# Kernel tuning notes

Measured on AMD Instinct MI355X. Metric: run time of the kernel, lower is better.

The kernel has to match this reference:

```python
import jax, jax.numpy as jnp
import numpy as np

TEMP = 0.1
W1, W2 = 0.5, 0.5
W3 = 1.0 - W1 - W2  # = 0.0, as in the original module defaults


def setup_inputs() -> dict:
    key = jax.random.key(0)
    ks = jax.random.split(key, 8)
    N, D = 131072, 256
    C1, C2, C3 = 1000, 100, 20
    features = jax.random.normal(ks[0], (N, D), dtype=jnp.float32) * 0.1
    prototypes_1 = jax.random.normal(ks[1], (C1, D), dtype=jnp.float32)
    labels_1 = jax.random.randint(ks[2], (N,), 0, C1)
    prototypes_2 = jax.random.normal(ks[3], (C2, D), dtype=jnp.float32)
    # ensure every coarse class appears (torch.unique == arange(C))
    labels_2 = jax.random.permutation(ks[4], jnp.arange(N) % C2)
    prototypes_3 = jax.random.normal(ks[5], (C3, D), dtype=jnp.float32)
    labels_3 = jax.random.permutation(ks[6], jnp.arange(N) % C3)
    return {
        "features": features,
        "prototypes_1": prototypes_1,
        "labels_1": labels_1,
        "prototypes_2": prototypes_2,
        "labels_2": labels_2,
        "prototypes_3": prototypes_3,
        "labels_3": labels_3,
    }


def _proto_nce(means, protos):
    # means: [C, D], protos: [C, D]; pos_mask(one_hot of unique=arange) is identity
    sim = (means @ protos.T) / TEMP              # [C, C]
    pos = jnp.diagonal(sim)                      # [C]
    return -jnp.mean(pos - jax.nn.logsumexp(sim, axis=1))


def _segment_mean(features, labels, num_segments):
    sums = jax.ops.segment_sum(features, labels, num_segments=num_segments)
    cnt = jax.ops.segment_sum(jnp.ones((labels.shape[0],), features.dtype),
                              labels, num_segments=num_segments)
    return sums / cnt[:, None]


def reference(features, prototypes_1, labels_1, prototypes_2, labels_2,
              prototypes_3, labels_3):
    # fine level: per-sample InfoNCE against fine prototypes
    fine_sim = (features @ prototypes_1.T) / TEMP            # [N, C1]
    fine_pos = jnp.take_along_axis(fine_sim, labels_1[:, None], axis=1)[:, 0]
    fine_loss = -jnp.mean(fine_pos - jax.nn.logsumexp(fine_sim, axis=1))

    # coarse level: per-class feature means (segment mean == masked-mean loop)
    coarse_means = _segment_mean(features, labels_2, prototypes_2.shape[0])
    coarse_loss = _proto_nce(coarse_means, prototypes_2)

    # con-coarse level
    con_means = _segment_mean(features, labels_3, prototypes_3.shape[0])
    con_coarse_loss = _proto_nce(con_means, prototypes_3)

    loss = W1 * fine_loss + W2 * coarse_loss + W3 * con_coarse_loss
    return (loss, fine_loss, coarse_loss, con_coarse_loss)
```

## Files before the change

kernel.cpp:

```cpp
#include <hip/hip_runtime.h>
#include <math.h>

#define WS_POS   0
#define WS_LSE   1
#define WS_ACC2  2
#define WS_ACC3  3
#define WS_S2    256
#define WS_S3    (256+25600)
#define WS_SEG   163840
#define NROWS    144
#define PART_FLOATS (NROWS*256 + 128)
#define PIMG_BYTE_OFF 131072

#define SC2  14.426950408889634f
#define BIAS 48.0f

typedef __attribute__((ext_vector_type(4))) float f32x4;
typedef __attribute__((ext_vector_type(8))) short short8;

static __device__ __forceinline__ unsigned f2bf(float f) {
    union { float f; unsigned u; } x; x.f = f;
    unsigned r = x.u + 0x7FFFu + ((x.u >> 16) & 1u);
    return r >> 16;
}

__global__ void k_zero(float* __restrict__ p, int count) {
    int i = blockIdx.x * 256 + threadIdx.x;
    if (i < count) p[i] = 0.f;
}

__global__ void k_prep(const float* __restrict__ p1, unsigned short* __restrict__ Pimg,
                       float* __restrict__ ws, int C1) {
    if (blockIdx.x == 0) ws[threadIdx.x] = 0.f;
    int e = blockIdx.x * 256 + threadIdx.x;
    int r  = e >> 5;
    int k0 = (e & 31) * 8;
    unsigned h[8];
#pragma unroll
    for (int j = 0; j < 8; ++j)
        h[j] = (r < C1) ? f2bf(p1[(size_t)r * 256 + k0 + j]) : 0u;
    uint4 v;
    v.x = h[0] | (h[1] << 16);
    v.y = h[2] | (h[3] << 16);
    v.z = h[4] | (h[5] << 16);
    v.w = h[6] | (h[7] << 16);
    *(uint4*)(Pimg + (size_t)r * 256 + k0) = v;
}

__global__ __launch_bounds__(256, 2) void k_seg(
        const float* __restrict__ feat, const float* __restrict__ p1,
        const int* __restrict__ l1, const int* __restrict__ l2,
        const int* __restrict__ l3, float* __restrict__ ws,
        int partMask, int useAtomic) {
    __shared__ int labs23[512];
    __shared__ int labs1[512];
    __shared__ float psum[4];
    const int tid  = threadIdx.x;
    const int lane = tid & 63;
    const int wv   = tid >> 6;
    const int g    = lane >> 4;
    const int rs   = lane & 15;
    const int chunk = blockIdx.x >> 1, half = blockIdx.x & 1;
    const int base  = chunk * 512;
    const int dimbase = half * 128 + wv * 32;

    for (int j = tid; j < 512; j += 256) {
        labs23[j] = l2[base + j] | (l3[base + j] << 16);
        labs1[j]  = l1[base + j];
    }
    __syncthreads();

    f32x4 acc[9][2];
#pragma unroll
    for (int mt = 0; mt < 9; ++mt)
#pragma unroll
        for (int nt = 0; nt < 2; ++nt) acc[mt][nt] = (f32x4){0.f, 0.f, 0.f, 0.f};

    float fA[16], pA[16], fB[16], pB[16];
    float posacc = 0.f;

#define LOADSTEP(u, F, P) { \
    const int sl0 = (u) * 32 + 8 * g; \
    _Pragma("unroll") \
    for (int j = 0; j < 8; ++j) { \
        const int sl = sl0 + j; \
        const size_t fb = (size_t)(base + sl) * 256 + dimbase + rs; \
        F[j]     = feat[fb]; \
        F[8 + j] = feat[fb + 16]; \
        const size_t pb = (size_t)labs1[sl] * 256 + dimbase + rs; \
        P[j]     = p1[pb]; \
        P[8 + j] = p1[pb + 16]; \
    } }

#define PROCSTEP(u, F, P) { \
    _Pragma("unroll") \
    for (int j = 0; j < 16; ++j) posacc = fmaf(F[j], P[j], posacc); \
    union { unsigned w[4]; short8 s; } b0, b1; \
    _Pragma("unroll") \
    for (int q = 0; q < 4; ++q) { \
        asm("v_cvt_pk_bf16_f32 %0, %1, %2" : "=v"(b0.w[q]) : "v"(F[2*q]),   "v"(F[2*q+1])); \
        asm("v_cvt_pk_bf16_f32 %0, %1, %2" : "=v"(b1.w[q]) : "v"(F[8+2*q]), "v"(F[8+2*q+1])); \
    } \
    int d2[8], d3[8]; \
    { const int sl0 = (u) * 32 + 8 * g; \
      _Pragma("unroll") \
      for (int j = 0; j < 8; ++j) { \
          const int v = labs23[sl0 + j]; \
          d2[j] = (v & 0xffff) - rs; \
          d3[j] = (v >> 16) - rs; \
      } } \
    _Pragma("unroll") \
    for (int mt = 0; mt < 7; ++mt) { \
        union { unsigned w[4]; short8 s; } af; \
        _Pragma("unroll") \
        for (int q = 0; q < 4; ++q) { \
            unsigned w = (d2[2*q] == mt*16) ? 0x3F80u : 0u; \
            if (d2[2*q+1] == mt*16) w |= 0x3F800000u; \
            af.w[q] = w; \
        } \
        acc[mt][0] = __builtin_amdgcn_mfma_f32_16x16x32_bf16(af.s, b0.s, acc[mt][0], 0, 0, 0); \
        acc[mt][1] = __builtin_amdgcn_mfma_f32_16x16x32_bf16(af.s, b1.s, acc[mt][1], 0, 0, 0); \
    } \
    _Pragma("unroll") \
    for (int mt = 0; mt < 2; ++mt) { \
        union { unsigned w[4]; short8 s; } af; \
        _Pragma("unroll") \
        for (int q = 0; q < 4; ++q) { \
            unsigned w = (d3[2*q] == mt*16) ? 0x3F80u : 0u; \
            if (d3[2*q+1] == mt*16) w |= 0x3F800000u; \
            af.w[q] = w; \
        } \
        acc[7+mt][0] = __builtin_amdgcn_mfma_f32_16x16x32_bf16(af.s, b0.s, acc[7+mt][0], 0, 0, 0); \
        acc[7+mt][1] = __builtin_amdgcn_mfma_f32_16x16x32_bf16(af.s, b1.s, acc[7+mt][1], 0, 0, 0); \
    } }

    LOADSTEP(0, fA, pA);
#pragma unroll 1
    for (int t = 0; t < 16; t += 2) {
        LOADSTEP(t + 1, fB, pB);
        PROCSTEP(t, fA, pA);
        if (t + 2 < 16) LOADSTEP(t + 2, fA, pA);
        PROCSTEP(t + 1, fB, pB);
    }
#undef LOADSTEP
#undef PROCSTEP

    float* part = ws + WS_SEG +
        (size_t)(useAtomic ? (chunk & partMask) : chunk) * PART_FLOATS;
#pragma unroll
    for (int mt = 0; mt < 9; ++mt)
#pragma unroll
        for (int nt = 0; nt < 2; ++nt)
#pragma unroll
            for (int r = 0; r < 4; ++r) {
                float v = acc[mt][nt][r];
                float* dst = &part[(mt * 16 + 4 * g + r) * 256 + dimbase + nt * 16 + rs];
                if (useAtomic) atomicAdd(dst, v); else *dst = v;
            }

    if (half == 0 && tid < 120) {
        float cnt = 0.f;
        const int isl2 = tid < 100;
        const int cls = isl2 ? tid : tid - 100;
#pragma unroll 8
        for (int j = 0; j < 512; ++j) {
            int v = labs23[j];
            int lab = isl2 ? (v & 0xffff) : (v >> 16);
            cnt += (lab == cls) ? 1.f : 0.f;
        }
        float* dst = &part[NROWS * 256 + tid];
        if (useAtomic) atomicAdd(dst, cnt); else *dst = cnt;
    }

#pragma unroll
    for (int m = 1; m < 64; m <<= 1) posacc += __shfl_xor(posacc, m);
    if (lane == 0) psum[wv] = posacc;
    __syncthreads();
    if (tid == 0) atomicAdd(&ws[WS_POS], psum[0] + psum[1] + psum[2] + psum[3]);
}

__global__ __launch_bounds__(256, 4) void k_div(float* __restrict__ ws, int npart) {
    __shared__ float cred[4];
    const int c = blockIdx.x;
    const int d = threadIdx.x;
    const int prow = (c < 100) ? c : 112 + (c - 100);
    float cv = (d < npart) ? ws[WS_SEG + (size_t)d * PART_FLOATS + NROWS * 256 + c] : 0.f;
#pragma unroll
    for (int m = 1; m < 64; m <<= 1) cv += __shfl_xor(cv, m);
    if ((d & 63) == 0) cred[d >> 6] = cv;
    __syncthreads();
    const float cnt = cred[0] + cred[1] + cred[2] + cred[3];
    float a0=0,a1=0,a2=0,a3=0,a4=0,a5=0,a6=0,a7=0;
    int p = 0;
    for (; p + 8 <= npart; p += 8) {
        const float* b = ws + WS_SEG + (size_t)p * PART_FLOATS + prow * 256 + d;
        a0 += b[0 * (size_t)PART_FLOATS];
        a1 += b[1 * (size_t)PART_FLOATS];
        a2 += b[2 * (size_t)PART_FLOATS];
        a3 += b[3 * (size_t)PART_FLOATS];
        a4 += b[4 * (size_t)PART_FLOATS];
        a5 += b[5 * (size_t)PART_FLOATS];
        a6 += b[6 * (size_t)PART_FLOATS];
        a7 += b[7 * (size_t)PART_FLOATS];
    }
    for (; p < npart; ++p)
        a0 += ws[WS_SEG + (size_t)p * PART_FLOATS + prow * 256 + d];
    const float s = ((a0+a1)+(a2+a3)) + ((a4+a5)+(a6+a7));
    ws[256 + ((c < 100) ? c * 256 : 25600 + (c - 100) * 256) + d] = s / cnt;
}

#define LOADB(dst, ptr, OFF) \
    asm volatile("global_load_dwordx4 %0, %1, off offset:" #OFF \
                 : "=v"(dst) : "v"(ptr))
#define LOADB8(buf, ptr) \
    LOADB(buf[0], ptr, 0);   LOADB(buf[1], ptr, 64);  \
    LOADB(buf[2], ptr, 128); LOADB(buf[3], ptr, 192); \
    LOADB(buf[4], ptr, 256); LOADB(buf[5], ptr, 320); \
    LOADB(buf[6], ptr, 384); LOADB(buf[7], ptr, 448)

__global__ __launch_bounds__(256, 2) void k_fine(
        const float* __restrict__ feat, const unsigned short* __restrict__ Pimg,
        float* __restrict__ ws, int C1) {
    __shared__ __align__(16) unsigned short Af[128 * 256];
    __shared__ float Sbuf[128];
    __shared__ float redl[2];
    const int tid  = threadIdx.x;
    const int lane = tid & 63;
    const int wv   = tid >> 6;
    const int g    = lane >> 4;
    const int rs   = lane & 15;
    const int row0 = blockIdx.x * 128;

#define PBP(p) ((const char*)Pimg + (size_t)((p) * 128 + wv * 32 + rs) * 512 + g * 16)

    short8 bA[2][8], bB[2][8];
    { const char* pb = PBP(0); LOADB8(bA[0], pb); LOADB8(bA[1], pb + 8192); }

#pragma unroll
    for (int i = 0; i < 16; ++i) {
        int u = tid + i * 256;
        int r = u >> 5, q8 = u & 31;
        const float* src = feat + (size_t)(row0 + r) * 256 + q8 * 8;
        f32x4 v0 = *(const f32x4*)(src);
        f32x4 v1 = *(const f32x4*)(src + 4);
        uint4 pk;
        asm("v_cvt_pk_bf16_f32 %0, %1, %2" : "=v"(pk.x) : "v"(v0[0]), "v"(v0[1]));
        asm("v_cvt_pk_bf16_f32 %0, %1, %2" : "=v"(pk.y) : "v"(v0[2]), "v"(v0[3]));
        asm("v_cvt_pk_bf16_f32 %0, %1, %2" : "=v"(pk.z) : "v"(v1[0]), "v"(v1[1]));
        asm("v_cvt_pk_bf16_f32 %0, %1, %2" : "=v"(pk.w) : "v"(v1[2]), "v"(v1[3]));
        *(uint4*)((char*)Af + r * 512 + ((q8 * 16) ^ ((r & 7) << 4))) = pk;
    }
    if (tid < 128) Sbuf[tid] = 0.f;
    __syncthreads();

    float es[8][4];
#pragma unroll
    for (int a = 0; a < 8; ++a)
#pragma unroll
        for (int b = 0; b < 4; ++b) es[a][b] = 0.f;

#define PASS(BUF, pp) { \
    _Pragma("unroll") \
    for (int rt = 0; rt < 8; ++rt) { \
        f32x4 acc0 = (f32x4){0.f, 0.f, 0.f, 0.f}; \
        f32x4 acc1 = (f32x4){0.f, 0.f, 0.f, 0.f}; \
        const int ar = rt * 16 + rs; \
        const char* abase = (const char*)Af + ar * 512; \
        const int sw = (ar & 7) << 4; \
        _Pragma("unroll") \
        for (int ks = 0; ks < 8; ++ks) { \
            short8 a = *(const short8*)(abase + ((ks * 64 + g * 16) ^ sw)); \
            acc0 = __builtin_amdgcn_mfma_f32_16x16x32_bf16(a, BUF[0][ks], acc0, 0, 0, 0); \
            acc1 = __builtin_amdgcn_mfma_f32_16x16x32_bf16(a, BUF[1][ks], acc1, 0, 0, 0); \
        } \
        _Pragma("unroll") \
        for (int r = 0; r < 4; ++r) { \
            float t0 = fmaf(acc0[r], SC2, -BIAS); \
            float t1 = fmaf(acc1[r], SC2, -BIAS); \
            float e0, e1; \
            asm("v_exp_f32 %0, %2\n\t" \
                "v_exp_f32 %1, %3\n\t" \
                "s_nop 1" \
                : "=&v"(e0), "=&v"(e1) : "v"(t0), "v"(t1)); \
            es[rt][r] += e0 + e1; \
        } \
    } }

#pragma unroll 1
    for (int p = 0; p < 8; p += 2) {
        { const char* pb = PBP(p + 1); LOADB8(bB[0], pb); LOADB8(bB[1], pb + 8192); }
        asm volatile("s_waitcnt vmcnt(16)" ::: "memory");
        __builtin_amdgcn_sched_barrier(0);
        PASS(bA, p);
        if (p + 2 < 8) {
            const char* pb = PBP(p + 2); LOADB8(bA[0], pb); LOADB8(bA[1], pb + 8192);
            asm volatile("s_waitcnt vmcnt(16)" ::: "memory");
        } else {
            asm volatile("s_waitcnt vmcnt(0)" ::: "memory");
        }
        __builtin_amdgcn_sched_barrier(0);
        PASS(bB, p + 1);
    }
#undef PASS
#undef PBP

#pragma unroll
    for (int rt = 0; rt < 8; ++rt) {
#pragma unroll
        for (int r = 0; r < 4; ++r) {
            float e = es[rt][r];
            e += __shfl_xor(e, 1);
            e += __shfl_xor(e, 2);
            e += __shfl_xor(e, 4);
            e += __shfl_xor(e, 8);
            if (rs == 0) atomicAdd(&Sbuf[rt * 16 + 4 * g + r], e);
        }
    }
    __syncthreads();
    if (tid < 128) {
        float S = Sbuf[tid] - (float)(1024 - C1) * exp2f(-BIAS);
        float lse = (BIAS + log2f(S)) * 0.6931471805599453f;
#pragma unroll
        for (int m = 1; m < 64; m <<= 1) lse += __shfl_xor(lse, m);
        if (lane == 0) redl[tid >> 6] = lse;
    }
    __syncthreads();
    if (tid == 0) atomicAdd(&ws[WS_LSE], redl[0] + redl[1]);
}

__global__ __launch_bounds__(128, 4) void k_nce(
        const float* __restrict__ p2, const float* __restrict__ p3,
        float* __restrict__ ws) {
    __shared__ __align__(16) float mrow[256];
    __shared__ float sim[128];
    __shared__ float red[2];
    const int b = blockIdx.x;
    const float* means; const float* prot; int C, r, accIdx;
    if (b < 100) { means = ws + WS_S2; prot = p2; C = 100; r = b;       accIdx = WS_ACC2; }
    else         { means = ws + WS_S3; prot = p3; C = 20;  r = b - 100; accIdx = WS_ACC3; }
    const int tid = threadIdx.x;
    const int lane = tid & 63;
    mrow[tid]       = means[(size_t)r * 256 + tid];
    mrow[128 + tid] = means[(size_t)r * 256 + 128 + tid];
    __syncthreads();
    if (tid < C) {
        const f32x4* mr = (const f32x4*)mrow;
        const f32x4* pr = (const f32x4*)(prot + (size_t)tid * 256);
        float acc = 0.f;
#pragma unroll 4
        for (int k = 0; k < 64; ++k) {
            f32x4 m = mr[k], qv = pr[k];
            acc += m[0]*qv[0] + m[1]*qv[1] + m[2]*qv[2] + m[3]*qv[3];
        }
        sim[tid] = acc * 10.0f;
    }
    __syncthreads();
    float v = (tid < C) ? sim[tid] : -1e30f;
#pragma unroll
    for (int m = 1; m < 64; m <<= 1) v = fmaxf(v, __shfl_xor(v, m));
    if (lane == 0) red[tid >> 6] = v;
    __syncthreads();
    const float mx = fmaxf(red[0], red[1]);
    float e = (tid < C) ? __expf(sim[tid] - mx) : 0.f;
#pragma unroll
    for (int m = 1; m < 64; m <<= 1) e += __shfl_xor(e, m);
    __syncthreads();
    if (lane == 0) red[tid >> 6] = e;
    __syncthreads();
    if (tid == 0) {
        float lse = mx + logf(red[0] + red[1]);
        atomicAdd(&ws[accIdx], lse - sim[r]);
    }
}

__global__ void k_final(const float* __restrict__ ws, float* __restrict__ out, float Nf) {
    if (threadIdx.x == 0 && blockIdx.x == 0) {
        float fine   = (ws[WS_LSE] - 10.0f * ws[WS_POS]) / Nf;
        float coarse = ws[WS_ACC2] / 100.0f;
        float con    = ws[WS_ACC3] / 20.0f;
        out[0] = 0.5f * fine + 0.5f * coarse + 0.0f * con;
        out[1] = fine;
        out[2] = coarse;
        out[3] = con;
    }
}

extern "C" void kernel_launch(void* const* d_in, const int* in_sizes, int n_in,
                              void* d_out, int out_size, void* d_ws, size_t ws_size,
                              hipStream_t stream) {
    const float* feat = (const float*)d_in[0];
    const float* p1   = (const float*)d_in[1];
    const int*   l1   = (const int*)d_in[2];
    const float* p2   = (const float*)d_in[3];
    const int*   l2   = (const int*)d_in[4];
    const float* p3   = (const float*)d_in[5];
    const int*   l3   = (const int*)d_in[6];
    float* out = (float*)d_out;
    float* ws  = (float*)d_ws;
    const int n  = in_sizes[0] / 256;
    const int c1 = in_sizes[1] / 256;
    unsigned short* Pimg = (unsigned short*)((char*)d_ws + PIMG_BYTE_OFF);

    const int nchunk = n / 512;
    long nfull = ((long)(ws_size / 4) - WS_SEG) / PART_FLOATS;
    int useAtomic, npart;
    if (nfull >= nchunk) { useAtomic = 0; npart = nchunk; }
    else {
        useAtomic = 1;
        npart = 1;
        while (npart * 2 <= (int)nfull && npart < 32) npart <<= 1;
    }

    if (useAtomic)
        k_zero <<<(npart * PART_FLOATS + 255) / 256, 256, 0, stream>>>(ws + WS_SEG, npart * PART_FLOATS);
    k_prep <<<128, 256, 0, stream>>>(p1, Pimg, ws, c1);
    k_seg  <<<nchunk * 2, 256, 0, stream>>>(feat, p1, l1, l2, l3, ws, npart - 1, useAtomic);
    k_div  <<<120, 256, 0, stream>>>(ws, npart);
    k_fine <<<n / 128, 256, 0, stream>>>(feat, Pimg, ws, c1);
    k_nce  <<<120, 128, 0, stream>>>(p2, p3, ws);
    k_final<<<1, 64, 0, stream>>>(ws, out, (float)n);
}
```

Before: 161.5 us.

## Merge segment-sum and fine-logits kernels into one interleaved launch

Combines k_seg and k_fine into one kernel whose blocks are interleaved: every third block runs the segment-sum body and the other two run the fine InfoNCE body, with both sharing one static LDS allocation. This removes a kernel launch boundary and lets the memory-bound segment work overlap with the MFMA-heavy fine work on the same CUs. The cost is that the segment blocks now reserve the large fine-kernel LDS footprint, and register pressure is set by the larger of the two bodies, which can reduce occupancy.

```diff
diff --git a/kernel.cpp b/kernel.cpp
--- a/kernel.cpp
+++ b/kernel.cpp
@@ -47,20 +47,27 @@
     *(uint4*)(Pimg + (size_t)r * 256 + k0) = v;
 }
 
-__global__ __launch_bounds__(256, 2) void k_seg(
+#define LOADB(dst, ptr, OFF) \
+    asm volatile("global_load_dwordx4 %0, %1, off offset:" #OFF \
+                 : "=v"(dst) : "v"(ptr))
+#define LOADB8(buf, ptr) \
+    LOADB(buf[0], ptr, 0);   LOADB(buf[1], ptr, 64);  \
+    LOADB(buf[2], ptr, 128); LOADB(buf[3], ptr, 192); \
+    LOADB(buf[4], ptr, 256); LOADB(buf[5], ptr, 320); \
+    LOADB(buf[6], ptr, 384); LOADB(buf[7], ptr, 448)
+
+static __device__ __forceinline__ void seg_body(
         const float* __restrict__ feat, const float* __restrict__ p1,
         const int* __restrict__ l1, const int* __restrict__ l2,
         const int* __restrict__ l3, float* __restrict__ ws,
-        int partMask, int useAtomic) {
-    __shared__ int labs23[512];
-    __shared__ int labs1[512];
-    __shared__ float psum[4];
+        int partMask, int useAtomic, int sblk,
+        int* labs23, int* labs1, float* psum) {
     const int tid  = threadIdx.x;
     const int lane = tid & 63;
     const int wv   = tid >> 6;
     const int g    = lane >> 4;
     const int rs   = lane & 15;
-    const int chunk = blockIdx.x >> 1, half = blockIdx.x & 1;
+    const int chunk = sblk >> 1, half = sblk & 1;
     const int base  = chunk * 512;
     const int dimbase = half * 128 + wv * 32;
 
@@ -179,57 +186,16 @@
     if (tid == 0) atomicAdd(&ws[WS_POS], psum[0] + psum[1] + psum[2] + psum[3]);
 }
 
-__global__ __launch_bounds__(256, 4) void k_div(float* __restrict__ ws, int npart) {
-    __shared__ float cred[4];
-    const int c = blockIdx.x;
-    const int d = threadIdx.x;
-    const int prow = (c < 100) ? c : 112 + (c - 100);
-    float cv = (d < npart) ? ws[WS_SEG + (size_t)d * PART_FLOATS + NROWS * 256 + c] : 0.f;
-#pragma unroll
-    for (int m = 1; m < 64; m <<= 1) cv += __shfl_xor(cv, m);
-    if ((d & 63) == 0) cred[d >> 6] = cv;
-    __syncthreads();
-    const float cnt = cred[0] + cred[1] + cred[2] + cred[3];
-    float a0=0,a1=0,a2=0,a3=0,a4=0,a5=0,a6=0,a7=0;
-    int p = 0;
-    for (; p + 8 <= npart; p += 8) {
-        const float* b = ws + WS_SEG + (size_t)p * PART_FLOATS + prow * 256 + d;
-        a0 += b[0 * (size_t)PART_FLOATS];
-        a1 += b[1 * (size_t)PART_FLOATS];
-        a2 += b[2 * (size_t)PART_FLOATS];
-        a3 += b[3 * (size_t)PART_FLOATS];
-        a4 += b[4 * (size_t)PART_FLOATS];
-        a5 += b[5 * (size_t)PART_FLOATS];
-        a6 += b[6 * (size_t)PART_FLOATS];
-        a7 += b[7 * (size_t)PART_FLOATS];
-    }
-    for (; p < npart; ++p)
-        a0 += ws[WS_SEG + (size_t)p * PART_FLOATS + prow * 256 + d];
-    const float s = ((a0+a1)+(a2+a3)) + ((a4+a5)+(a6+a7));
-    ws[256 + ((c < 100) ? c * 256 : 25600 + (c - 100) * 256) + d] = s / cnt;
-}
-
-#define LOADB(dst, ptr, OFF) \
-    asm volatile("global_load_dwordx4 %0, %1, off offset:" #OFF \
-                 : "=v"(dst) : "v"(ptr))
-#define LOADB8(buf, ptr) \
-    LOADB(buf[0], ptr, 0);   LOADB(buf[1], ptr, 64);  \
-    LOADB(buf[2], ptr, 128); LOADB(buf[3], ptr, 192); \
-    LOADB(buf[4], ptr, 256); LOADB(buf[5], ptr, 320); \
-    LOADB(buf[6], ptr, 384); LOADB(buf[7], ptr, 448)
-
-__global__ __launch_bounds__(256, 2) void k_fine(
+static __device__ __forceinline__ void fine_body(
         const float* __restrict__ feat, const unsigned short* __restrict__ Pimg,
-        float* __restrict__ ws, int C1) {
-    __shared__ __align__(16) unsigned short Af[128 * 256];
-    __shared__ float Sbuf[128];
-    __shared__ float redl[2];
+        float* __restrict__ ws, int C1, int fblk,
+        unsigned short* Af, float* Sbuf, float* redl) {
     const int tid  = threadIdx.x;
     const int lane = tid & 63;
     const int wv   = tid >> 6;
     const int g    = lane >> 4;
     const int rs   = lane & 15;
-    const int row0 = blockIdx.x * 128;
+    const int row0 = fblk * 128;
 
 #define PBP(p) ((const char*)Pimg + (size_t)((p) * 128 + wv * 32 + rs) * 512 + g * 16)
 
@@ -328,6 +294,55 @@
     if (tid == 0) atomicAdd(&ws[WS_LSE], redl[0] + redl[1]);
 }
 
+__global__ __launch_bounds__(256, 2) void k_merged(
+        const float* __restrict__ feat, const float* __restrict__ p1,
+        const unsigned short* __restrict__ Pimg,
+        const int* __restrict__ l1, const int* __restrict__ l2,
+        const int* __restrict__ l3, float* __restrict__ ws,
+        int C1, int partMask, int useAtomic) {
+    __shared__ __align__(16) unsigned short Af[128 * 256];
+    __shared__ float Sbuf[128];
+    __shared__ float redl[2];
+    const int bid = blockIdx.x;
+    if (bid % 3 == 0) {
+        seg_body(feat, p1, l1, l2, l3, ws, partMask, useAtomic, bid / 3,
+                 (int*)Af, (int*)(Af + 1024), Sbuf);
+    } else {
+        fine_body(feat, Pimg, ws, C1, (bid - 1) - (bid - 1) / 3,
+                  Af, Sbuf, redl);
+    }
+}
+
+__global__ __launch_bounds__(256, 4) void k_div(float* __restrict__ ws, int npart) {
+    __shared__ float cred[4];
+    const int c = blockIdx.x;
+    const int d = threadIdx.x;
+    const int prow = (c < 100) ? c : 112 + (c - 100);
+    float cv = (d < npart) ? ws[WS_SEG + (size_t)d * PART_FLOATS + NROWS * 256 + c] : 0.f;
+#pragma unroll
+    for (int m = 1; m < 64; m <<= 1) cv += __shfl_xor(cv, m);
+    if ((d & 63) == 0) cred[d >> 6] = cv;
+    __syncthreads();
+    const float cnt = cred[0] + cred[1] + cred[2] + cred[3];
+    float a0=0,a1=0,a2=0,a3=0,a4=0,a5=0,a6=0,a7=0;
+    int p = 0;
+    for (; p + 8 <= npart; p += 8) {
+        const float* b = ws + WS_SEG + (size_t)p * PART_FLOATS + prow * 256 + d;
+        a0 += b[0 * (size_t)PART_FLOATS];
+        a1 += b[1 * (size_t)PART_FLOATS];
+        a2 += b[2 * (size_t)PART_FLOATS];
+        a3 += b[3 * (size_t)PART_FLOATS];
+        a4 += b[4 * (size_t)PART_FLOATS];
+        a5 += b[5 * (size_t)PART_FLOATS];
+        a6 += b[6 * (size_t)PART_FLOATS];
+        a7 += b[7 * (size_t)PART_FLOATS];
+    }
+    for (; p < npart; ++p)
+        a0 += ws[WS_SEG + (size_t)p * PART_FLOATS + prow * 256 + d];
+    const float s = ((a0+a1)+(a2+a3)) + ((a4+a5)+(a6+a7));
+    ws[256 + ((c < 100) ? c * 256 : 25600 + (c - 100) * 256) + d] = s / cnt;
+}
+
 __global__ __launch_bounds__(128, 4) void k_nce(
         const float* __restrict__ p2, const float* __restrict__ p3,
         float* __restrict__ ws) {
@@ -414,9 +429,9 @@
     if (useAtomic)
         k_zero <<<(npart * PART_FLOATS + 255) / 256, 256, 0, stream>>>(ws + WS_SEG, npart * PART_FLOATS);
     k_prep <<<128, 256, 0, stream>>>(p1, Pimg, ws, c1);
-    k_seg  <<<nchunk * 2, 256, 0, stream>>>(feat, p1, l1, l2, l3, ws, npart - 1, useAtomic);
+    k_merged <<<nchunk * 6, 256, 0, stream>>>(feat, p1, Pimg, l1, l2, l3, ws,
+                                              c1, npart - 1, useAtomic);
     k_div  <<<120, 256, 0, stream>>>(ws, npart);
-    k_fine <<<n / 128, 256, 0, stream>>>(feat, Pimg, ws, c1);
     k_nce  <<<120, 128, 0, stream>>>(p2, p3, ws);
     k_final<<<1, 64, 0, stream>>>(ws, out, (float)n);
 }
```

New measurement: 154.4 us. -4.4%, faster.
